# Kernel optimization log

Measured on AMD Instinct MI355X. Metric: run time of the kernel, lower is better.

## Reference

```python
import jax, jax.numpy as jnp
import numpy as np

B, N, C = 2, 384, 1024          # images, proposals/image, box_head feature dim
H_REPN = 256                    # RePN hidden
G_HID, HEADS = 256, 4           # GATConv hidden / heads
TOPK = 8
IMG_H, IMG_W = 800, 800
NEG_SLOPE = 0.2                 # PyG GATConv leaky_relu default


def _box_geom(bx):
    # normalized [x, y, w, h], matching _box_geom
    scale = jnp.array([IMG_W, IMG_H, IMG_W, IMG_H], dtype=bx.dtype)
    nb = bx / scale
    return jnp.stack([nb[:, 0], nb[:, 1], nb[:, 2] - nb[:, 0], nb[:, 3] - nb[:, 1]], axis=1)


def _gat_layer(x, src, tgt, W, att_src, att_dst, bias, heads, out_c):
    # PyG GATConv: messages flow src -> tgt, softmax over incoming edges at tgt
    n = x.shape[0]
    xw = (x @ W).reshape(n, heads, out_c)               # [N, H, F]
    a_s = jnp.sum(xw * att_src, axis=-1)                # [N, H]
    a_d = jnp.sum(xw * att_dst, axis=-1)                # [N, H]
    e = jax.nn.leaky_relu(a_s[src] + a_d[tgt], NEG_SLOPE)  # [E, H]
    e_max = jax.ops.segment_max(e, tgt, num_segments=n)    # stable softmax per target
    alpha = jnp.exp(e - e_max[tgt])
    denom = jax.ops.segment_sum(alpha, tgt, num_segments=n)
    alpha = alpha / jnp.maximum(denom, 1e-16)[tgt]          # [E, H]
    out = jax.ops.segment_sum(xw[src] * alpha[..., None], tgt, num_segments=n)
    return out.reshape(n, heads * out_c) + bias


def setup_inputs() -> dict:
    key = jax.random.key(0)
    ks = jax.random.split(key, 16)
    feats = jax.random.normal(ks[0], (B, N, C), dtype=jnp.float32)
    # boxes with x1<x2, y1<y2 inside the image
    xy = jax.random.uniform(ks[1], (B, N, 2), minval=0.0, maxval=650.0)
    wh = jax.random.uniform(ks[2], (B, N, 2), minval=10.0, maxval=150.0)
    boxes = jnp.concatenate([xy, xy + wh], axis=-1).astype(jnp.float32)
    s = 0.02
    params = {
        'fc1_w': jax.random.normal(ks[3], (2 * C + 4, H_REPN)) * s,
        'fc1_b': jnp.zeros((H_REPN,), jnp.float32),
        'fc2_w': jax.random.normal(ks[4], (H_REPN, 1)) * s,
        'fc2_b': jnp.zeros((1,), jnp.float32),
        'gat1_w': jax.random.normal(ks[5], (C + 4, HEADS * G_HID)) * s,
        'gat1_att_src': jax.random.normal(ks[6], (HEADS, G_HID)) * s,
        'gat1_att_dst': jax.random.normal(ks[7], (HEADS, G_HID)) * s,
        'gat1_b': jnp.zeros((HEADS * G_HID,), jnp.float32),
        'gat2_w': jax.random.normal(ks[8], (HEADS * G_HID, 2)) * s,
        'gat2_att_src': jax.random.normal(ks[9], (1, 2)) * s,
        'gat2_att_dst': jax.random.normal(ks[10], (1, 2)) * s,
        'gat2_b': jnp.zeros((2,), jnp.float32),
    }
    return {'feats': feats, 'boxes': boxes, **params}


def reference(feats, boxes, fc1_w, fc1_b, fc2_w, fc2_b,
              gat1_w, gat1_att_src, gat1_att_dst, gat1_b,
              gat2_w, gat2_att_src, gat2_att_dst, gat2_b):
    def single(f, bx):
        geom4 = _box_geom(bx)                               # [N, 4]
        x = jnp.concatenate([f, geom4], axis=1)             # [N, C+4]
        # RelationProposalNetwork: fc1(cat[f_i, f_j, |b_i-b_j|]) done as split matmuls
        Wa, Wb, Wg = fc1_w[:C], fc1_w[C:2 * C], fc1_w[2 * C:]
        p1 = f @ Wa                                         # [N, H]
        p2 = f @ Wb                                         # [N, H]
        gdiff = jnp.abs(bx[:, None, :] - bx[None, :, :])    # [N, N, 4]
        h = jax.nn.relu(p1[:, None, :] + p2[None, :, :] + gdiff @ Wg + fc1_b)
        rel = (h @ fc2_w)[..., 0] + fc2_b[0]                # [N, N]
        # _make_edge_index: mask diagonal, top-k per row; edge = [dst_node, neighbor]
        rn = rel - jnp.eye(N, dtype=rel.dtype) * 1e6
        nbr = jax.lax.top_k(rn, TOPK)[1]                    # [N, k]
        src = jnp.repeat(jnp.arange(N), TOPK)               # edge_index[0] (PyG source)
        tgt = nbr.reshape(-1)                               # edge_index[1] (PyG target)
        loop = jnp.arange(N)                                # GATConv add_self_loops=True
        src = jnp.concatenate([src, loop])
        tgt = jnp.concatenate([tgt, loop])
        h1 = jax.nn.relu(_gat_layer(x, src, tgt, gat1_w, gat1_att_src, gat1_att_dst, gat1_b, HEADS, G_HID))
        logits = _gat_layer(h1, src, tgt, gat2_w, gat2_att_src, gat2_att_dst, gat2_b, 1, 2)
        return logits                                       # [N, 2]
    return jax.vmap(single)(feats, boxes)
```

## Files before the change

### kernel.cpp

```cpp
#include <hip/hip_runtime.h>

#define BB 2
#define NN 384
#define CC 1024
#define HR 256
#define NHEADS 4
#define TOPK 8
#define CAP 448
#define NEG 0.2f

typedef __attribute__((ext_vector_type(8))) short bf16x8;
typedef __attribute__((ext_vector_type(4))) float f32x4;

__device__ __forceinline__ unsigned short f2bf(float v) {
    unsigned u = __float_as_uint(v);
    return (unsigned short)((u + 0x7FFFu + ((u >> 16) & 1u)) >> 16);
}
__device__ __forceinline__ float bf2f(unsigned short h) {
    return __uint_as_float((unsigned)h << 16);
}

__global__ __launch_bounds__(256) void k_prep(const float* __restrict__ feats,
        const float* __restrict__ boxes, const float* __restrict__ gat1_w,
        const float* __restrict__ fc1_w,
        uint4* __restrict__ Asw, uint4* __restrict__ Bsw,
        uint4* __restrict__ Ah, uint4* __restrict__ Al,
        uint4* __restrict__ Bh, uint4* __restrict__ Bl,
        float4* __restrict__ wgp, int* __restrict__ counts) {
    __shared__ float sw[32][65];
    int blk = blockIdx.x;
    int t = threadIdx.x;
    int gflat = blk * 256 + t;
    if (gflat < BB * NN) counts[gflat] = 0;

    if (blk < 396) {
        int flat = gflat;
        int lane = flat & 63;
        int kc = (flat >> 6) % 33;
        int mt = flat / (33 * 64);
        int m = mt * 16 + (lane & 15);
        int k0 = kc * 32 + (lane >> 4) * 8;
        unsigned short vals[8];
        const float s = 1.0f / 800.0f;
#pragma unroll
        for (int j = 0; j < 8; j++) {
            int k = k0 + j;
            float v;
            if (k < CC) v = feats[(size_t)m * CC + k];
            else if (k < CC + 4) {
                const float* bx = boxes + (size_t)m * 4;
                int gk = k - CC;
                v = (gk == 0) ? bx[0] * s : (gk == 1) ? bx[1] * s
                  : (gk == 2) ? (bx[2] - bx[0]) * s : (bx[3] - bx[1]) * s;
            } else v = 0.f;
            vals[j] = f2bf(v);
        }
        uint4 pk;
        pk.x = (unsigned)vals[0] | ((unsigned)vals[1] << 16);
        pk.y = (unsigned)vals[2] | ((unsigned)vals[3] << 16);
        pk.z = (unsigned)vals[4] | ((unsigned)vals[5] << 16);
        pk.w = (unsigned)vals[6] | ((unsigned)vals[7] << 16);
        Asw[flat] = pk;
    } else if (blk < 924) {
        int blkrel = blk - 396;
        int ntg = blkrel / 33;
        int kc  = blkrel % 33;
        int k0 = kc * 32;
        int n0 = ntg * 64;
#pragma unroll
        for (int pass = 0; pass < 8; pass++) {
            int kl = pass * 4 + (t >> 6);
            int k = k0 + kl;
            int nl = t & 63;
            float v = (k < CC + 4) ? gat1_w[(size_t)k * 1024 + n0 + nl] : 0.f;
            sw[kl][nl] = v;
        }
        __syncthreads();
        int local_nt = t >> 6;
        int lane = t & 63;
        int nn = lane & 15;
        int q = lane >> 4;
        int nl = local_nt * 16 + nn;
        unsigned short vals[8];
#pragma unroll
        for (int j = 0; j < 8; j++) vals[j] = f2bf(sw[q * 8 + j][nl]);
        uint4 pk;
        pk.x = (unsigned)vals[0] | ((unsigned)vals[1] << 16);
        pk.y = (unsigned)vals[2] | ((unsigned)vals[3] << 16);
        pk.z = (unsigned)vals[4] | ((unsigned)vals[5] << 16);
        pk.w = (unsigned)vals[6] | ((unsigned)vals[7] << 16);
        int nt = ntg * 4 + local_nt;
        Bsw[(size_t)nt * 33 * 64 + kc * 64 + lane] = pk;
    } else if (blk < 1308) {
        int flat = gflat - 924 * 256;
        int lane = flat & 63;
        int kc = (flat >> 6) % 32;
        int mt = flat / (32 * 64);
        int m = mt * 16 + (lane & 15);
        int k0 = kc * 32 + (lane >> 4) * 8;
        unsigned short vh[8], vl[8];
        const float* src = feats + (size_t)m * CC + k0;
#pragma unroll
        for (int j = 0; j < 8; j++) {
            float v = src[j];
            unsigned short h = f2bf(v);
            vh[j] = h;
            vl[j] = f2bf(v - bf2f(h));
        }
        uint4 ph, pl;
        ph.x = (unsigned)vh[0] | ((unsigned)vh[1] << 16);
        ph.y = (unsigned)vh[2] | ((unsigned)vh[3] << 16);
        ph.z = (unsigned)vh[4] | ((unsigned)vh[5] << 16);
        ph.w = (unsigned)vh[6] | ((unsigned)vh[7] << 16);
        pl.x = (unsigned)vl[0] | ((unsigned)vl[1] << 16);
        pl.y = (unsigned)vl[2] | ((unsigned)vl[3] << 16);
        pl.z = (unsigned)vl[4] | ((unsigned)vl[5] << 16);
        pl.w = (unsigned)vl[6] | ((unsigned)vl[7] << 16);
        Ah[flat] = ph; Al[flat] = pl;
    } else if (blk < 1564) {
        int blkrel = blk - 1308;
        int ntg = blkrel / 32;
        int kc  = blkrel % 32;
        int k0 = kc * 32;
        int n0 = ntg * 64;
#pragma unroll
        for (int pass = 0; pass < 8; pass++) {
            int kl = pass * 4 + (t >> 6);
            int k = k0 + kl;
            int n = n0 + (t & 63);
            float v = (n < 256) ? fc1_w[(size_t)k * 256 + n]
                                : fc1_w[(size_t)(CC + k) * 256 + (n - 256)];
            sw[kl][t & 63] = v;
        }
        __syncthreads();
        int local_nt = t >> 6;
        int lane = t & 63;
        int nn = lane & 15;
        int q = lane >> 4;
        int nl = local_nt * 16 + nn;
        unsigned short vh[8], vl[8];
#pragma unroll
        for (int j = 0; j < 8; j++) {
            float v = sw[q * 8 + j][nl];
            unsigned short h = f2bf(v);
            vh[j] = h;
            vl[j] = f2bf(v - bf2f(h));
        }
        uint4 ph, pl;
        ph.x = (unsigned)vh[0] | ((unsigned)vh[1] << 16);
        ph.y = (unsigned)vh[2] | ((unsigned)vh[3] << 16);
        ph.z = (unsigned)vh[4] | ((unsigned)vh[5] << 16);
        ph.w = (unsigned)vh[6] | ((unsigned)vh[7] << 16);
        pl.x = (unsigned)vl[0] | ((unsigned)vl[1] << 16);
        pl.y = (unsigned)vl[2] | ((unsigned)vl[3] << 16);
        pl.z = (unsigned)vl[4] | ((unsigned)vl[5] << 16);
        pl.w = (unsigned)vl[6] | ((unsigned)vl[7] << 16);
        int nt = ntg * 4 + local_nt;
        size_t o = (size_t)nt * 32 * 64 + kc * 64 + lane;
        Bh[o] = ph; Bl[o] = pl;
    } else {
        int c = t;
        float4 w;
        w.x = fc1_w[(size_t)(2 * CC + 0) * HR + c];
        w.y = fc1_w[(size_t)(2 * CC + 1) * HR + c];
        w.z = fc1_w[(size_t)(2 * CC + 2) * HR + c];
        w.w = fc1_w[(size_t)(2 * CC + 3) * HR + c];
        wgp[c] = w;
    }
}

__global__ __launch_bounds__(512) void k_mm(const uint4* __restrict__ Ah,
        const uint4* __restrict__ Al, const uint4* __restrict__ Bh,
        const uint4* __restrict__ Bl, const float* __restrict__ fc1_b,
        float* __restrict__ p1, float* __restrict__ p2t,
        const uint4* __restrict__ Asw, const uint4* __restrict__ Bsw,
        float* __restrict__ xw1) {
    __shared__ float lds[4][64][8];
    int t = threadIdx.x;
    int w = t >> 6;
    int lane = t & 63;
    int g = w & 3;
    int kh = w >> 2;
    int blk0 = blockIdx.x;
    if (blk0 < 192) {
        int mtp = blk0 >> 3;
        int nt = (blk0 & 7) * 4 + g;
        int mt0 = mtp * 2;
        f32x4 acc0 = {0.f, 0.f, 0.f, 0.f};
        f32x4 acc1 = {0.f, 0.f, 0.f, 0.f};
        const uint4* pah0 = Ah + (size_t)mt0 * 32 * 64 + (size_t)kh * 16 * 64 + lane;
        const uint4* pal0 = Al + (size_t)mt0 * 32 * 64 + (size_t)kh * 16 * 64 + lane;
        const uint4* pbh = Bh + (size_t)nt * 32 * 64 + (size_t)kh * 16 * 64 + lane;
        const uint4* pbl = Bl + (size_t)nt * 32 * 64 + (size_t)kh * 16 * 64 + lane;
#pragma unroll 2
        for (int kc = 0; kc < 16; kc++) {
            uint4 ah0 = pah0[kc * 64];
            uint4 al0 = pal0[kc * 64];
            uint4 ah1 = pah0[kc * 64 + 2048];
            uint4 al1 = pal0[kc * 64 + 2048];
            uint4 bh = pbh[kc * 64];
            uint4 bl = pbl[kc * 64];
            acc0 = __builtin_amdgcn_mfma_f32_16x16x32_bf16(*(bf16x8*)&ah0, *(bf16x8*)&bh, acc0, 0, 0, 0);
            acc0 = __builtin_amdgcn_mfma_f32_16x16x32_bf16(*(bf16x8*)&ah0, *(bf16x8*)&bl, acc0, 0, 0, 0);
            acc0 = __builtin_amdgcn_mfma_f32_16x16x32_bf16(*(bf16x8*)&al0, *(bf16x8*)&bh, acc0, 0, 0, 0);
            acc1 = __builtin_amdgcn_mfma_f32_16x16x32_bf16(*(bf16x8*)&ah1, *(bf16x8*)&bh, acc1, 0, 0, 0);
            acc1 = __builtin_amdgcn_mfma_f32_16x16x32_bf16(*(bf16x8*)&ah1, *(bf16x8*)&bl, acc1, 0, 0, 0);
            acc1 = __builtin_amdgcn_mfma_f32_16x16x32_bf16(*(bf16x8*)&al1, *(bf16x8*)&bh, acc1, 0, 0, 0);
        }
        if (kh == 1) {
#pragma unroll
            for (int r = 0; r < 4; r++) { lds[g][lane][r] = acc0[r]; lds[g][lane][4 + r] = acc1[r]; }
        }
        __syncthreads();
        if (kh == 0) {
#pragma unroll
            for (int r = 0; r < 4; r++) { acc0[r] += lds[g][lane][r]; acc1[r] += lds[g][lane][4 + r]; }
            int col = nt * 16 + (lane & 15);
            int rbase = (lane >> 4) * 4;
            if (col < 256) {
                float bias = fc1_b[col];
#pragma unroll
                for (int r = 0; r < 4; r++) {
                    p1[(size_t)(mt0 * 16 + rbase + r) * 256 + col] = acc0[r] + bias;
                    p1[(size_t)(mt0 * 16 + 16 + rbase + r) * 256 + col] = acc1[r] + bias;
                }
            } else {
#pragma unroll
                for (int r = 0; r < 4; r++) {
                    int rr0 = mt0 * 16 + rbase + r;
                    int rr1 = rr0 + 16;
                    p2t[((size_t)(rr0 / NN) * 256 + (col - 256)) * NN + (rr0 % NN)] = acc0[r];
                    p2t[((size_t)(rr1 / NN) * 256 + (col - 256)) * NN + (rr1 % NN)] = acc1[r];
                }
            }
        }
    } else {
        int blk = blk0 - 192;
        int mtp = blk >> 4;
        int nt = (blk & 15) * 4 + g;
        int mt0 = mtp * 2;
        int nk = kh ? 16 : 17;
        f32x4 acc0 = {0.f, 0.f, 0.f, 0.f};
        f32x4 acc1 = {0.f, 0.f, 0.f, 0.f};
        const uint4* pa0 = Asw + (size_t)mt0 * 33 * 64 + (size_t)kh * 17 * 64 + lane;
        const uint4* pb = Bsw + (size_t)nt * 33 * 64 + (size_t)kh * 17 * 64 + lane;
#pragma unroll 4
        for (int kc = 0; kc < nk; kc++) {
            uint4 a0 = pa0[kc * 64];
            uint4 a1 = pa0[kc * 64 + 2112];
            uint4 bv = pb[kc * 64];
            acc0 = __builtin_amdgcn_mfma_f32_16x16x32_bf16(*(bf16x8*)&a0, *(bf16x8*)&bv, acc0, 0, 0, 0);
            acc1 = __builtin_amdgcn_mfma_f32_16x16x32_bf16(*(bf16x8*)&a1, *(bf16x8*)&bv, acc1, 0, 0, 0);
        }
        if (kh == 1) {
#pragma unroll
            for (int r = 0; r < 4; r++) { lds[g][lane][r] = acc0[r]; lds[g][lane][4 + r] = acc1[r]; }
        }
        __syncthreads();
        if (kh == 0) {
#pragma unroll
            for (int r = 0; r < 4; r++) { acc0[r] += lds[g][lane][r]; acc1[r] += lds[g][lane][4 + r]; }
            int col = nt * 16 + (lane & 15);
            int rbase = (lane >> 4) * 4;
#pragma unroll
            for (int r = 0; r < 4; r++) {
                xw1[(size_t)(mt0 * 16 + rbase + r) * 1024 + col] = acc0[r];
                xw1[(size_t)(mt0 * 16 + 16 + rbase + r) * 1024 + col] = acc1[r];
            }
        }
    }
}

__global__ __launch_bounds__(384) void k_relatt(const float* __restrict__ p1,
        const float* __restrict__ p2t, const float* __restrict__ boxes,
        const float4* __restrict__ wgp, const float* __restrict__ fc2_w,
        float* __restrict__ relq,
        const float* __restrict__ xw1, const float* __restrict__ att_src,
        const float* __restrict__ att_dst, float* __restrict__ a_s,
        float* __restrict__ a_d) {
    int blk0 = blockIdx.x;
    if (blk0 < 768) {
        int b = blk0 / 384;
        int rem = blk0 - b * 384;
        int q = rem & 3;
        int rg = rem >> 2;
        int i0 = rg * 4;
        int row0 = b * NN + i0;
        int j = threadIdx.x;
        float4 br0 = *(const float4*)(boxes + (size_t)row0 * 4);
        float4 br1 = *(const float4*)(boxes + (size_t)(row0 + 1) * 4);
        float4 br2 = *(const float4*)(boxes + (size_t)(row0 + 2) * 4);
        float4 br3 = *(const float4*)(boxes + (size_t)(row0 + 3) * 4);
        float4 bj = *(const float4*)(boxes + ((size_t)b * NN + j) * 4);
        float g00 = fabsf(br0.x - bj.x), g01 = fabsf(br0.y - bj.y);
        float g02 = fabsf(br0.z - bj.z), g03 = fabsf(br0.w - bj.w);
        float g10 = fabsf(br1.x - bj.x), g11 = fabsf(br1.y - bj.y);
        float g12 = fabsf(br1.z - bj.z), g13 = fabsf(br1.w - bj.w);
        float g20 = fabsf(br2.x - bj.x), g21 = fabsf(br2.y - bj.y);
        float g22 = fabsf(br2.z - bj.z), g23 = fabsf(br2.w - bj.w);
        float g30 = fabsf(br3.x - bj.x), g31 = fabsf(br3.y - bj.y);
        float g32 = fabsf(br3.z - bj.z), g33 = fabsf(br3.w - bj.w);
        const float* p1b = p1 + (size_t)row0 * HR + q * 64;
        const float* p2b = p2t + (size_t)b * HR * NN + (size_t)(q * 64) * NN + j;
        const float4* wg = wgp + q * 64;
        const float* w2 = fc2_w + q * 64;
        float acc0 = 0.f, acc1 = 0.f, acc2 = 0.f, acc3 = 0.f;
#pragma unroll 4
        for (int c = 0; c < 64; c++) {
            float4 w = wg[c];
            float wc = w2[c];
            float pa0 = p1b[c];
            float pa1 = p1b[c + HR];
            float pa2 = p1b[c + 2 * HR];
            float pa3 = p1b[c + 3 * HR];
            float p2v = p2b[(size_t)c * NN];
            float v0 = pa0 + p2v + g00 * w.x + g01 * w.y + g02 * w.z + g03 * w.w;
            float v1 = pa1 + p2v + g10 * w.x + g11 * w.y + g12 * w.z + g13 * w.w;
            float v2 = pa2 + p2v + g20 * w.x + g21 * w.y + g22 * w.z + g23 * w.w;
            float v3 = pa3 + p2v + g30 * w.x + g31 * w.y + g32 * w.z + g33 * w.w;
            acc0 += fmaxf(v0, 0.f) * wc;
            acc1 += fmaxf(v1, 0.f) * wc;
            acc2 += fmaxf(v2, 0.f) * wc;
            acc3 += fmaxf(v3, 0.f) * wc;
        }
        float* dst = relq + ((size_t)q * (BB * NN) + row0) * NN + j;
        dst[0]          = acc0;
        dst[NN]         = acc1;
        dst[2 * NN]     = acc2;
        dst[3 * (size_t)NN] = acc3;
    } else {
        int node = blk0 - 768;
        int t = threadIdx.x;
        if (t >= 256) return;
        int w = t >> 6;
        int lane = t & 63;
        const float4* xr = (const float4*)(xw1 + (size_t)node * 1024 + w * 256);
        const float4* sr = (const float4*)(att_src + w * 256);
        const float4* dr = (const float4*)(att_dst + w * 256);
        float4 x = xr[lane];
        float4 s = sr[lane];
        float4 d = dr[lane];
        float ps = x.x * s.x + x.y * s.y + x.z * s.z + x.w * s.w;
        float pd = x.x * d.x + x.y * d.y + x.z * d.z + x.w * d.w;
#pragma unroll
        for (int off = 32; off > 0; off >>= 1) {
            ps += __shfl_xor(ps, off);
            pd += __shfl_xor(pd, off);
        }
        if (lane == 0) {
            a_s[(size_t)node * NHEADS + w] = ps;
            a_d[(size_t)node * NHEADS + w] = pd;
        }
    }
}

__global__ __launch_bounds__(64) void k_topk_inv(const float* __restrict__ relq,
        int* __restrict__ counts, int* __restrict__ inlist) {
    int row = blockIdx.x;
    int b = row / NN;
    int i = row - b * NN;
    int t = threadIdx.x;
    const float* r0 = relq + (size_t)row * NN;
    const float* r1 = r0 + (size_t)(BB * NN) * NN;
    const float* r2 = r1 + (size_t)(BB * NN) * NN;
    const float* r3 = r2 + (size_t)(BB * NN) * NN;
    float v[6]; int id[6];
#pragma unroll
    for (int q = 0; q < 6; q++) {
        int j = t + q * 64;
        float val = ((r0[j] + r1[j]) + r2[j]) + r3[j];
        if (j == i) val = -INFINITY;
        v[q] = val; id[q] = j;
    }
    int mine = -1;
    for (int k = 0; k < TOPK; k++) {
        float bv = -INFINITY; int bi = NN;
#pragma unroll
        for (int q = 0; q < 6; q++) {
            if (v[q] > bv || (v[q] == bv && id[q] < bi)) { bv = v[q]; bi = id[q]; }
        }
        for (int off = 32; off > 0; off >>= 1) {
            float ov = __shfl_down(bv, off);
            int   oi = __shfl_down(bi, off);
            if (ov > bv || (ov == bv && oi < bi)) { bv = ov; bi = oi; }
        }
        bi = __shfl(bi, 0);
        if (t == k) mine = bi;
#pragma unroll
        for (int q = 0; q < 6; q++) if (id[q] == bi) v[q] = -INFINITY;
    }
    if (t < TOPK) {
        int tg = b * NN + mine;
        int q = atomicAdd(&counts[tg], 1);
        inlist[(size_t)tg * CAP + q] = i;
    } else if (t == TOPK) {
        int q = atomicAdd(&counts[row], 1);
        inlist[(size_t)row * CAP + q] = i;
    }
}

__global__ __launch_bounds__(512) void k_agg1(const int* __restrict__ counts,
        const int* __restrict__ inlist, const float* __restrict__ a_s,
        const float* __restrict__ a_d, const float* __restrict__ xw1,
        const float* __restrict__ gat1_b, const float* __restrict__ w2,
        float* __restrict__ xw2) {
    __shared__ int slist[CAP];
    __shared__ float walpha[NHEADS][CAP];
    __shared__ float redp[16];
    int node = blockIdx.x;
    int b = node / NN;
    int t = threadIdx.x;
    int wid = t >> 6;
    int lane = t & 63;
    int deg = counts[node];
    for (int e = t; e < deg; e += 512) slist[e] = inlist[(size_t)node * CAP + e];
    __syncthreads();
    if (t < 256) {
        int h = wid;
        float ad = a_d[(size_t)node * NHEADS + h];
        float vals[7];
        int cnt = 0;
        float vmax = -INFINITY;
        for (int e = lane; e < deg; e += 64) {
            float x = a_s[(size_t)(b * NN + slist[e]) * NHEADS + h] + ad;
            x = x >= 0.f ? x : NEG * x;
            vals[cnt++] = x;
            vmax = fmaxf(vmax, x);
        }
#pragma unroll
        for (int off = 32; off > 0; off >>= 1)
            vmax = fmaxf(vmax, __shfl_xor(vmax, off));
        float sum = 0.f;
        for (int i = 0; i < cnt; i++) {
            vals[i] = expf(vals[i] - vmax);
            sum += vals[i];
        }
#pragma unroll
        for (int off = 32; off > 0; off >>= 1)
            sum += __shfl_xor(sum, off);
        float inv = 1.f / fmaxf(sum, 1e-16f);
        cnt = 0;
        for (int e = lane; e < deg; e += 64) walpha[h][e] = vals[cnt++] * inv;
    }
    __syncthreads();
    int d0 = t, d1 = t + 512;
    int h0 = d0 >> 8, h1 = d1 >> 8;
    float acc0 = 0.f, acc1 = 0.f;
    for (int e = 0; e < deg; e++) {
        const float* xr = xw1 + (size_t)(b * NN + slist[e]) * 1024;
        acc0 += walpha[h0][e] * xr[d0];
        acc1 += walpha[h1][e] * xr[d1];
    }
    float o0 = fmaxf(acc0 + gat1_b[d0], 0.f);
    float o1 = fmaxf(acc1 + gat1_b[d1], 0.f);
    float p0 = o0 * w2[d0 * 2]     + o1 * w2[d1 * 2];
    float p1v = o0 * w2[d0 * 2 + 1] + o1 * w2[d1 * 2 + 1];
#pragma unroll
    for (int off = 32; off > 0; off >>= 1) {
        p0 += __shfl_xor(p0, off);
        p1v += __shfl_xor(p1v, off);
    }
    if (lane == 0) { redp[wid] = p0; redp[8 + wid] = p1v; }
    __syncthreads();
    if (t == 0) {
        float s0 = 0.f, s1 = 0.f;
#pragma unroll
        for (int q = 0; q < 8; q++) { s0 += redp[q]; s1 += redp[8 + q]; }
        xw2[(size_t)node * 2]     = s0;
        xw2[(size_t)node * 2 + 1] = s1;
    }
}

__global__ __launch_bounds__(64) void k_agg2(const int* __restrict__ counts,
        const int* __restrict__ inlist, const float* __restrict__ xw2,
        const float* __restrict__ as2, const float* __restrict__ ad2,
        const float* __restrict__ b2, float* __restrict__ out) {
    int node = blockIdx.x;
    int b = node / NN;
    int lane = threadIdx.x;
    int deg = counts[node];
    float s0 = as2[0], s1 = as2[1];
    float d0 = ad2[0], d1 = ad2[1];
    float2 xwn = *(const float2*)(xw2 + (size_t)node * 2);
    float ad = xwn.x * d0 + xwn.y * d1;
    float vals[7], xs0[7], xs1[7];
    int cnt = 0;
    float vmax = -INFINITY;
    for (int e = lane; e < deg; e += 64) {
        int s = b * NN + inlist[(size_t)node * CAP + e];
        float2 xws = *(const float2*)(xw2 + (size_t)s * 2);
        float x = xws.x * s0 + xws.y * s1 + ad;
        x = x >= 0.f ? x : NEG * x;
        xs0[cnt] = xws.x; xs1[cnt] = xws.y; vals[cnt] = x; cnt++;
        vmax = fmaxf(vmax, x);
    }
#pragma unroll
    for (int off = 32; off > 0; off >>= 1)
        vmax = fmaxf(vmax, __shfl_xor(vmax, off));
    float sum = 0.f;
    for (int i = 0; i < cnt; i++) {
        vals[i] = expf(vals[i] - vmax);
        sum += vals[i];
    }
#pragma unroll
    for (int off = 32; off > 0; off >>= 1)
        sum += __shfl_xor(sum, off);
    float inv = 1.f / fmaxf(sum, 1e-16f);
    float a0 = 0.f, a1 = 0.f;
    for (int i = 0; i < cnt; i++) {
        a0 += vals[i] * xs0[i];
        a1 += vals[i] * xs1[i];
    }
#pragma unroll
    for (int off = 32; off > 0; off >>= 1) {
        a0 += __shfl_xor(a0, off);
        a1 += __shfl_xor(a1, off);
    }
    if (lane == 0) {
        out[(size_t)node * 2]     = a0 * inv + b2[0];
        out[(size_t)node * 2 + 1] = a1 * inv + b2[1];
    }
}

extern "C" void kernel_launch(void* const* d_in, const int* in_sizes, int n_in,
                              void* d_out, int out_size, void* d_ws, size_t ws_size,
                              hipStream_t stream) {
    const float* feats  = (const float*)d_in[0];
    const float* boxes  = (const float*)d_in[1];
    const float* fc1_w  = (const float*)d_in[2];
    const float* fc1_b  = (const float*)d_in[3];
    const float* fc2_w  = (const float*)d_in[4];
    const float* fc2_b  = (const float*)d_in[5];
    const float* gat1_w = (const float*)d_in[6];
    const float* g1as   = (const float*)d_in[7];
    const float* g1ad   = (const float*)d_in[8];
    const float* gat1_b = (const float*)d_in[9];
    const float* gat2_w = (const float*)d_in[10];
    const float* g2as   = (const float*)d_in[11];
    const float* g2ad   = (const float*)d_in[12];
    const float* gat2_b = (const float*)d_in[13];
    float* out = (float*)d_out;
    (void)fc2_b;

    char* ws = (char*)d_ws;
    size_t off = 0;
    auto alloc = [&](size_t bytes) -> void* {
        void* p = ws + off;
        off += (bytes + 255) / 256 * 256;
        return p;
    };
    int*   counts = (int*)alloc((size_t)BB * NN * 4);
    int*   inlist = (int*)alloc((size_t)BB * NN * CAP * 4);
    float* p1     = (float*)alloc((size_t)BB * NN * HR * 4);
    float* p2t    = (float*)alloc((size_t)BB * HR * NN * 4);
    float* relq   = (float*)alloc((size_t)4 * BB * NN * NN * 4);
    float* xw1    = (float*)alloc((size_t)BB * NN * 1024 * 4);
    float* a_s1   = (float*)alloc((size_t)BB * NN * NHEADS * 4);
    float* a_d1   = (float*)alloc((size_t)BB * NN * NHEADS * 4);
    float* xw2    = (float*)alloc((size_t)BB * NN * 2 * 4);
    uint4* Asw    = (uint4*)alloc((size_t)48 * 33 * 64 * 16);
    uint4* Bsw    = (uint4*)alloc((size_t)64 * 33 * 64 * 16);
    uint4* Ah     = (uint4*)alloc((size_t)48 * 32 * 64 * 16);
    uint4* Al     = (uint4*)alloc((size_t)48 * 32 * 64 * 16);
    uint4* Bh     = (uint4*)alloc((size_t)32 * 32 * 64 * 16);
    uint4* Bl     = (uint4*)alloc((size_t)32 * 32 * 64 * 16);
    float4* wgp   = (float4*)alloc((size_t)HR * 16);
    (void)ws_size; (void)in_sizes; (void)n_in; (void)out_size;

    k_prep<<<1565, 256, 0, stream>>>(feats, boxes, gat1_w, fc1_w,
                                     Asw, Bsw, Ah, Al, Bh, Bl, wgp, counts);
    k_mm<<<576, 512, 0, stream>>>(Ah, Al, Bh, Bl, fc1_b, p1, p2t, Asw, Bsw, xw1);
    k_relatt<<<1536, 384, 0, stream>>>(p1, p2t, boxes, wgp, fc2_w, relq,
                                       xw1, g1as, g1ad, a_s1, a_d1);
    k_topk_inv<<<BB * NN, 64, 0, stream>>>(relq, counts, inlist);
    k_agg1<<<BB * NN, 512, 0, stream>>>(counts, inlist, a_s1, a_d1, xw1,
                                        gat1_b, gat2_w, xw2);
    k_agg2<<<BB * NN, 64, 0, stream>>>(counts, inlist, xw2, g2as, g2ad, gat2_b, out);
}
```

Baseline: 160.8 us.

## Retile projection GEMMs into larger LDS-staged, double-buffered block tiles

Replaces the per-wave direct-from-global MFMA GEMM, which split K across two wave groups and reduced through LDS, with larger block tiles (128 rows by 64 or 128 columns). A and B fragments are staged through double-buffered LDS and shared by all waves. The aim is to cut redundant global loads of operand fragments by reusing them across waves. In exchange the grid shrinks from 576 to 96 blocks, which lowers occupancy and parallelism on a many-CU GPU, and the loop adds two barriers per K step.

```diff
diff --git a/kernel.cpp b/kernel.cpp
--- a/kernel.cpp
+++ b/kernel.cpp
@@ -169,103 +169,136 @@
     }
 }
 
-__global__ __launch_bounds__(512) void k_mm(const uint4* __restrict__ Ah,
+__global__ __launch_bounds__(512) void k_mm2(const uint4* __restrict__ Ah,
         const uint4* __restrict__ Al, const uint4* __restrict__ Bh,
         const uint4* __restrict__ Bl, const float* __restrict__ fc1_b,
         float* __restrict__ p1, float* __restrict__ p2t,
         const uint4* __restrict__ Asw, const uint4* __restrict__ Bsw,
         float* __restrict__ xw1) {
-    __shared__ float lds[4][64][8];
+    __shared__ uint4 lbuf[2][1536];
     int t = threadIdx.x;
-    int w = t >> 6;
-    int lane = t & 63;
-    int g = w & 3;
-    int kh = w >> 2;
+    int w = t >> 6, lane = t & 63;
     int blk0 = blockIdx.x;
-    if (blk0 < 192) {
-        int mtp = blk0 >> 3;
-        int nt = (blk0 & 7) * 4 + g;
-        int mt0 = mtp * 2;
-        f32x4 acc0 = {0.f, 0.f, 0.f, 0.f};
-        f32x4 acc1 = {0.f, 0.f, 0.f, 0.f};
-        const uint4* pah0 = Ah + (size_t)mt0 * 32 * 64 + (size_t)kh * 16 * 64 + lane;
-        const uint4* pal0 = Al + (size_t)mt0 * 32 * 64 + (size_t)kh * 16 * 64 + lane;
-        const uint4* pbh = Bh + (size_t)nt * 32 * 64 + (size_t)kh * 16 * 64 + lane;
-        const uint4* pbl = Bl + (size_t)nt * 32 * 64 + (size_t)kh * 16 * 64 + lane;
-#pragma unroll 2
-        for (int kc = 0; kc < 16; kc++) {
-            uint4 ah0 = pah0[kc * 64];
-            uint4 al0 = pal0[kc * 64];
-            uint4 ah1 = pah0[kc * 64 + 2048];
-            uint4 al1 = pal0[kc * 64 + 2048];
-            uint4 bh = pbh[kc * 64];
-            uint4 bl = pbl[kc * 64];
-            acc0 = __builtin_amdgcn_mfma_f32_16x16x32_bf16(*(bf16x8*)&ah0, *(bf16x8*)&bh, acc0, 0, 0, 0);
-            acc0 = __builtin_amdgcn_mfma_f32_16x16x32_bf16(*(bf16x8*)&ah0, *(bf16x8*)&bl, acc0, 0, 0, 0);
-            acc0 = __builtin_amdgcn_mfma_f32_16x16x32_bf16(*(bf16x8*)&al0, *(bf16x8*)&bh, acc0, 0, 0, 0);
-            acc1 = __builtin_amdgcn_mfma_f32_16x16x32_bf16(*(bf16x8*)&ah1, *(bf16x8*)&bh, acc1, 0, 0, 0);
-            acc1 = __builtin_amdgcn_mfma_f32_16x16x32_bf16(*(bf16x8*)&ah1, *(bf16x8*)&bl, acc1, 0, 0, 0);
-            acc1 = __builtin_amdgcn_mfma_f32_16x16x32_bf16(*(bf16x8*)&al1, *(bf16x8*)&bh, acc1, 0, 0, 0);
-        }
-        if (kh == 1) {
-#pragma unroll
-            for (int r = 0; r < 4; r++) { lds[g][lane][r] = acc0[r]; lds[g][lane][4 + r] = acc1[r]; }
-        }
+    if (blk0 < 48) {
+        int bm = blk0 >> 3, bn = blk0 & 7;
+        f32x4 acc[4];
+#pragma unroll
+        for (int j = 0; j < 4; j++) acc[j] = (f32x4){0.f, 0.f, 0.f, 0.f};
+        const uint4* sb[3];
+        int ldsrow[3];
+#pragma unroll
+        for (int q = 0; q < 3; q++) {
+            int r = w * 3 + q;
+            ldsrow[q] = r * 64 + lane;
+            if (r < 16) {
+                int mtl = r >> 1, hl = r & 1;
+                sb[q] = (hl ? Al : Ah) + (size_t)(bm * 8 + mtl) * 32 * 64 + lane;
+            } else {
+                int rb = r - 16;
+                int ntl = rb >> 1, hl = rb & 1;
+                sb[q] = (hl ? Bl : Bh) + (size_t)(bn * 4 + ntl) * 32 * 64 + lane;
+            }
+        }
+        uint4 regs[3];
+#pragma unroll
+        for (int q = 0; q < 3; q++) regs[q] = sb[q][0];
+#pragma unroll
+        for (int q = 0; q < 3; q++) lbuf[0][ldsrow[q]] = regs[q];
         __syncthreads();
-        if (kh == 0) {
-#pragma unroll
-            for (int r = 0; r < 4; r++) { acc0[r] += lds[g][lane][r]; acc1[r] += lds[g][lane][4 + r]; }
-            int col = nt * 16 + (lane & 15);
-            int rbase = (lane >> 4) * 4;
+        for (int kc = 0; kc < 32; kc++) {
+            const uint4* lb = lbuf[kc & 1];
+            if (kc < 31) {
+#pragma unroll
+                for (int q = 0; q < 3; q++) regs[q] = sb[q][(kc + 1) * 64];
+            }
+            uint4 a_h = lb[(2 * w) * 64 + lane];
+            uint4 a_l = lb[(2 * w + 1) * 64 + lane];
+#pragma unroll
+            for (int ntl = 0; ntl < 4; ntl++) {
+                uint4 b_h = lb[(16 + 2 * ntl) * 64 + lane];
+                uint4 b_l = lb[(16 + 2 * ntl + 1) * 64 + lane];
+                acc[ntl] = __builtin_amdgcn_mfma_f32_16x16x32_bf16(*(bf16x8*)&a_h, *(bf16x8*)&b_h, acc[ntl], 0, 0, 0);
+                acc[ntl] = __builtin_amdgcn_mfma_f32_16x16x32_bf16(*(bf16x8*)&a_h, *(bf16x8*)&b_l, acc[ntl], 0, 0, 0);
+                acc[ntl] = __builtin_amdgcn_mfma_f32_16x16x32_bf16(*(bf16x8*)&a_l, *(bf16x8*)&b_h, acc[ntl], 0, 0, 0);
+            }
+            __syncthreads();
+            if (kc < 31) {
+#pragma unroll
+                for (int q = 0; q < 3; q++) lbuf[(kc & 1) ^ 1][ldsrow[q]] = regs[q];
+                __syncthreads();
+            }
+        }
+        int colb = lane & 15;
+        int rbase = (lane >> 4) * 4;
+        int mt = bm * 8 + w;
+#pragma unroll
+        for (int ntl = 0; ntl < 4; ntl++) {
+            int col = (bn * 4 + ntl) * 16 + colb;
             if (col < 256) {
                 float bias = fc1_b[col];
 #pragma unroll
                 for (int r = 0; r < 4; r++) {
-                    p1[(size_t)(mt0 * 16 + rbase + r) * 256 + col] = acc0[r] + bias;
-                    p1[(size_t)(mt0 * 16 + 16 + rbase + r) * 256 + col] = acc1[r] + bias;
+                    int rr = mt * 16 + rbase + r;
+                    p1[(size_t)rr * 256 + col] = acc[ntl][r] + bias;
                 }
             } else {
 #pragma unroll
                 for (int r = 0; r < 4; r++) {
-                    int rr0 = mt0 * 16 + rbase + r;
-                    int rr1 = rr0 + 16;
-                    p2t[((size_t)(rr0 / NN) * 256 + (col - 256)) * NN + (rr0 % NN)] = acc0[r];
-                    p2t[((size_t)(rr1 / NN) * 256 + (col - 256)) * NN + (rr1 % NN)] = acc1[r];
+                    int rr = mt * 16 + rbase + r;
+                    p2t[((size_t)(rr / NN) * 256 + (col - 256)) * NN + (rr % NN)] = acc[ntl][r];
                 }
             }
         }
     } else {
-        int blk = blk0 - 192;
-        int mtp = blk >> 4;
-        int nt = (blk & 15) * 4 + g;
-        int mt0 = mtp * 2;
-        int nk = kh ? 16 : 17;
-        f32x4 acc0 = {0.f, 0.f, 0.f, 0.f};
-        f32x4 acc1 = {0.f, 0.f, 0.f, 0.f};
-        const uint4* pa0 = Asw + (size_t)mt0 * 33 * 64 + (size_t)kh * 17 * 64 + lane;
-        const uint4* pb = Bsw + (size_t)nt * 33 * 64 + (size_t)kh * 17 * 64 + lane;
-#pragma unroll 4
-        for (int kc = 0; kc < nk; kc++) {
-            uint4 a0 = pa0[kc * 64];
-            uint4 a1 = pa0[kc * 64 + 2112];
-            uint4 bv = pb[kc * 64];
-            acc0 = __builtin_amdgcn_mfma_f32_16x16x32_bf16(*(bf16x8*)&a0, *(bf16x8*)&bv, acc0, 0, 0, 0);
-            acc1 = __builtin_amdgcn_mfma_f32_16x16x32_bf16(*(bf16x8*)&a1, *(bf16x8*)&bv, acc1, 0, 0, 0);
-        }
-        if (kh == 1) {
-#pragma unroll
-            for (int r = 0; r < 4; r++) { lds[g][lane][r] = acc0[r]; lds[g][lane][4 + r] = acc1[r]; }
-        }
+        int blk = blk0 - 48;
+        int bm = blk >> 3, bn = blk & 7;
+        f32x4 acc[8];
+#pragma unroll
+        for (int j = 0; j < 8; j++) acc[j] = (f32x4){0.f, 0.f, 0.f, 0.f};
+        const uint4* sb[2];
+        int ldsrow[2];
+#pragma unroll
+        for (int q = 0; q < 2; q++) {
+            int r = w * 2 + q;
+            ldsrow[q] = r * 64 + lane;
+            if (r < 8) sb[q] = Asw + (size_t)(bm * 8 + r) * 33 * 64 + lane;
+            else       sb[q] = Bsw + (size_t)(bn * 8 + (r - 8)) * 33 * 64 + lane;
+        }
+        uint4 regs[2];
+#pragma unroll
+        for (int q = 0; q < 2; q++) regs[q] = sb[q][0];
+#pragma unroll
+        for (int q = 0; q < 2; q++) lbuf[0][ldsrow[q]] = regs[q];
         __syncthreads();
-        if (kh == 0) {
-#pragma unroll
-            for (int r = 0; r < 4; r++) { acc0[r] += lds[g][lane][r]; acc1[r] += lds[g][lane][4 + r]; }
-            int col = nt * 16 + (lane & 15);
-            int rbase = (lane >> 4) * 4;
+        for (int kc = 0; kc < 33; kc++) {
+            const uint4* lb = lbuf[kc & 1];
+            if (kc < 32) {
+#pragma unroll
+                for (int q = 0; q < 2; q++) regs[q] = sb[q][(kc + 1) * 64];
+            }
+            uint4 av = lb[w * 64 + lane];
+#pragma unroll
+            for (int ntl = 0; ntl < 8; ntl++) {
+                uint4 bv = lb[(8 + ntl) * 64 + lane];
+                acc[ntl] = __builtin_amdgcn_mfma_f32_16x16x32_bf16(*(bf16x8*)&av, *(bf16x8*)&bv, acc[ntl], 0, 0, 0);
+            }
+            __syncthreads();
+            if (kc < 32) {
+#pragma unroll
+                for (int q = 0; q < 2; q++) lbuf[(kc & 1) ^ 1][ldsrow[q]] = regs[q];
+                __syncthreads();
+            }
+        }
+        int colb = lane & 15;
+        int rbase = (lane >> 4) * 4;
+        int mt = bm * 8 + w;
+#pragma unroll
+        for (int ntl = 0; ntl < 8; ntl++) {
+            int col = (bn * 8 + ntl) * 16 + colb;
 #pragma unroll
             for (int r = 0; r < 4; r++) {
-                xw1[(size_t)(mt0 * 16 + rbase + r) * 1024 + col] = acc0[r];
-                xw1[(size_t)(mt0 * 16 + 16 + rbase + r) * 1024 + col] = acc1[r];
+                int rr = mt * 16 + rbase + r;
+                xw1[(size_t)rr * 1024 + col] = acc[ntl][r];
             }
         }
     }
@@ -569,7 +602,7 @@
 
     k_prep<<<1565, 256, 0, stream>>>(feats, boxes, gat1_w, fc1_w,
                                      Asw, Bsw, Ah, Al, Bh, Bl, wgp, counts);
-    k_mm<<<576, 512, 0, stream>>>(Ah, Al, Bh, Bl, fc1_b, p1, p2t, Asw, Bsw, xw1);
+    k_mm2<<<96, 512, 0, stream>>>(Ah, Al, Bh, Bl, fc1_b, p1, p2t, Asw, Bsw, xw1);
     k_relatt<<<1536, 384, 0, stream>>>(p1, p2t, boxes, wgp, fc2_w, relq,
                                        xw1, g1as, g1ad, a_s1, a_d1);
     k_topk_inv<<<BB * NN, 64, 0, stream>>>(relq, counts, inlist);
```

After: 209.4 us. 30.3% more time.
